# Kernel tuning notes

Hardware: AMD Instinct MI355X
Metric: run time of the kernel (lower is better)

## Reference

```python
import jax, jax.numpy as jnp
import numpy as np

EMBED_DIM = 1024
NUM_HEADS = 16
SEQ_LEN = 2048
BATCH = 2
LN_EPS = 1e-5


def setup_inputs() -> dict:
    key = jax.random.key(0)
    ks = jax.random.split(key, 12)
    d = EMBED_DIM
    s = 1.0 / np.sqrt(d)
    inp = {
        "x": jax.random.normal(ks[0], (BATCH, SEQ_LEN, d), dtype=jnp.float32),
        "ln1_g": jnp.ones((d,), jnp.float32),
        "ln1_b": jnp.zeros((d,), jnp.float32),
        "ln2_g": jnp.ones((d,), jnp.float32),
        "ln2_b": jnp.zeros((d,), jnp.float32),
        "W_qkv": jax.random.normal(ks[1], (d, 3 * d), jnp.float32) * s,
        "b_qkv": jnp.zeros((3 * d,), jnp.float32),
        "W_proj": jax.random.normal(ks[2], (d, d), jnp.float32) * s,
        "b_proj": jnp.zeros((d,), jnp.float32),
        "W_fc": jax.random.normal(ks[3], (d, 4 * d), jnp.float32) * s,
        "b_fc": jnp.zeros((4 * d,), jnp.float32),
        "W_out": jax.random.normal(ks[4], (4 * d, d), jnpp_dummy := jnp.float32) * (1.0 / np.sqrt(4 * d)),
        "b_out": jnp.zeros((d,), jnp.float32),
    }
    return inp


def _layernorm(x, g, b):
    mu = jnp.mean(x, axis=-1, keepdims=True)
    var = jnp.mean(jnp.square(x - mu), axis=-1, keepdims=True)
    return (x - mu) * jax.lax.rsqrt(var + LN_EPS) * g + b


def _block(x, ln1_g, ln1_b, ln2_g, ln2_b, W_qkv, b_qkv, W_proj, b_proj, W_fc, b_fc, W_out, b_out):
    B, S, D = x.shape
    H = NUM_HEADS
    hd = D // H
    h = _layernorm(x, ln1_g, ln1_b)
    qkv = h @ W_qkv + b_qkv  # [B,S,3D]
    q, k, v = jnp.split(qkv, 3, axis=-1)
    # [B,H,S,hd]
    q = q.reshape(B, S, H, hd).transpose(0, 2, 1, 3)
    k = k.reshape(B, S, H, hd).transpose(0, 2, 1, 3)
    v = v.reshape(B, S, H, hd).transpose(0, 2, 1, 3)
    attn = jnp.einsum("bhqd,bhkd->bhqk", q, k) / np.sqrt(hd).astype(np.float32)
    causal = jnp.tril(jnp.ones((S, S), dtype=bool))
    attn = jnp.where(causal, attn, -jnp.inf)
    attn = jax.nn.softmax(attn, axis=-1)
    y = jnp.einsum("bhqk,bhkd->bhqd", attn, v)
    y = y.transpose(0, 2, 1, 3).reshape(B, S, D)
    y = y @ W_proj + b_proj
    x = x + y
    h2 = _layernorm(x, ln2_g, ln2_b)
    m = jax.nn.relu(h2 @ W_fc + b_fc) @ W_out + b_out
    return x + m


def reference(x, ln1_g, ln1_b, ln2_g, ln2_b, W_qkv, b_qkv, W_proj, b_proj, W_fc, b_fc, W_out, b_out):
    return _block(x, ln1_g, ln1_b, ln2_g, ln2_b, W_qkv, b_qkv, W_proj, b_proj, W_fc, b_fc, W_out, b_out)
```

## Files before the change

### kernel.cpp

```cpp
#include <hip/hip_runtime.h>

typedef unsigned short u16;
typedef __attribute__((ext_vector_type(8))) __bf16 bf16x8;
typedef __attribute__((ext_vector_type(4))) float f32x4;

#define DEV __device__ __forceinline__

DEV u16 f2bf(float f) {
  unsigned u = __float_as_uint(f);
  u += 0x7fffu + ((u >> 16) & 1u);
  return (u16)(u >> 16);
}
DEV float bf2f(u16 u) { return __uint_as_float((unsigned)u << 16); }

DEV void gl_lds16(const void* g, void* l) {
  __builtin_amdgcn_global_load_lds(
      (const __attribute__((address_space(1))) void*)(uintptr_t)g,
      (__attribute__((address_space(3))) void*)(unsigned)(uintptr_t)l, 16, 0, 0);
}

DEV float wave_sum64(float v) {
#pragma unroll
  for (int off = 32; off > 0; off >>= 1) v += __shfl_down(v, off);
  return v;
}

__global__ __launch_bounds__(256) void ln_kernel(const float* __restrict__ x,
                                                 const float* __restrict__ g,
                                                 const float* __restrict__ be,
                                                 u16* __restrict__ out) {
  const int row = blockIdx.x, t = threadIdx.x;
  const int w = t >> 6, L = t & 63;
  __shared__ float red[8];
  const float4 v = reinterpret_cast<const float4*>(x + (size_t)row * 1024)[t];
  float s = v.x + v.y + v.z + v.w;
  s = wave_sum64(s);
  if (L == 0) red[w] = s;
  __syncthreads();
  const float mean = (red[0] + red[1] + red[2] + red[3]) * (1.0f / 1024.0f);
  const float dx = v.x - mean, dy = v.y - mean, dz = v.z - mean, dw = v.w - mean;
  float q = dx * dx + dy * dy + dz * dz + dw * dw;
  q = wave_sum64(q);
  if (L == 0) red[4 + w] = q;
  __syncthreads();
  const float var = (red[4] + red[5] + red[6] + red[7]) * (1.0f / 1024.0f);
  const float rs = rsqrtf(var + 1e-5f);
  const float4 gg = reinterpret_cast<const float4*>(g)[t];
  const float4 bb = reinterpret_cast<const float4*>(be)[t];
  ushort4 o;
  o.x = f2bf(dx * rs * gg.x + bb.x);
  o.y = f2bf(dy * rs * gg.y + bb.y);
  o.z = f2bf(dz * rs * gg.z + bb.z);
  o.w = f2bf(dw * rs * gg.w + bb.w);
  reinterpret_cast<ushort4*>(out + (size_t)row * 1024)[t] = o;
}

__global__ __launch_bounds__(256) void proj_reduce_ln(const float* __restrict__ x,
                                                      const float* __restrict__ bias,
                                                      const float* __restrict__ P,
                                                      const float* __restrict__ g,
                                                      const float* __restrict__ be,
                                                      float* __restrict__ x2,
                                                      u16* __restrict__ hbuf) {
  constexpr size_t MN = (size_t)4096 * 1024;
  const int row = blockIdx.x, t = threadIdx.x;
  const int w = t >> 6, L = t & 63;
  __shared__ float red[8];
  const float4 xv = reinterpret_cast<const float4*>(x + (size_t)row * 1024)[t];
  const float4 bv = reinterpret_cast<const float4*>(bias)[t];
  const float4 p0 = reinterpret_cast<const float4*>(P + (size_t)row * 1024)[t];
  const float4 p1 = reinterpret_cast<const float4*>(P + MN + (size_t)row * 1024)[t];
  float4 v;
  v.x = xv.x + bv.x + p0.x + p1.x;
  v.y = xv.y + bv.y + p0.y + p1.y;
  v.z = xv.z + bv.z + p0.z + p1.z;
  v.w = xv.w + bv.w + p0.w + p1.w;
  reinterpret_cast<float4*>(x2 + (size_t)row * 1024)[t] = v;
  float s = v.x + v.y + v.z + v.w;
  s = wave_sum64(s);
  if (L == 0) red[w] = s;
  __syncthreads();
  const float mean = (red[0] + red[1] + red[2] + red[3]) * (1.0f / 1024.0f);
  const float dx = v.x - mean, dy = v.y - mean, dz = v.z - mean, dw = v.w - mean;
  float q = dx * dx + dy * dy + dz * dz + dw * dw;
  q = wave_sum64(q);
  if (L == 0) red[4 + w] = q;
  __syncthreads();
  const float var = (red[4] + red[5] + red[6] + red[7]) * (1.0f / 1024.0f);
  const float rs = rsqrtf(var + 1e-5f);
  const float4 gg = reinterpret_cast<const float4*>(g)[t];
  const float4 bb = reinterpret_cast<const float4*>(be)[t];
  ushort4 o;
  o.x = f2bf(dx * rs * gg.x + bb.x);
  o.y = f2bf(dy * rs * gg.y + bb.y);
  o.z = f2bf(dz * rs * gg.z + bb.z);
  o.w = f2bf(dw * rs * gg.w + bb.w);
  reinterpret_cast<ushort4*>(hbuf + (size_t)row * 1024)[t] = o;
}

__global__ __launch_bounds__(256) void out_reduce(const float* __restrict__ x2,
                                                  const float* __restrict__ bias,
                                                  const u16* __restrict__ P0,
                                                  const u16* __restrict__ P1,
                                                  const u16* __restrict__ P2,
                                                  const u16* __restrict__ P3,
                                                  float* __restrict__ dout) {
  const int row = blockIdx.x, t = threadIdx.x;
  const size_t off = (size_t)row * 1024;
  const float4 xv = reinterpret_cast<const float4*>(x2 + off)[t];
  const float4 bv = reinterpret_cast<const float4*>(bias)[t];
  const ushort4 a = reinterpret_cast<const ushort4*>(P0 + off)[t];
  const ushort4 b = reinterpret_cast<const ushort4*>(P1 + off)[t];
  const ushort4 c = reinterpret_cast<const ushort4*>(P2 + off)[t];
  const ushort4 d = reinterpret_cast<const ushort4*>(P3 + off)[t];
  float4 o;
  o.x = xv.x + bv.x + bf2f(a.x) + bf2f(b.x) + bf2f(c.x) + bf2f(d.x);
  o.y = xv.y + bv.y + bf2f(a.y) + bf2f(b.y) + bf2f(c.y) + bf2f(d.y);
  o.z = xv.z + bv.z + bf2f(a.z) + bf2f(b.z) + bf2f(c.z) + bf2f(d.z);
  o.w = xv.w + bv.w + bf2f(a.w) + bf2f(b.w) + bf2f(c.w) + bf2f(d.w);
  reinterpret_cast<float4*>(dout + off)[t] = o;
}

__global__ __launch_bounds__(256) void transpose_cvt(const float* __restrict__ W,
                                                     u16* __restrict__ Wt, int K, int N) {
  __shared__ float tile[32][33];
  const int c0 = blockIdx.x * 32, r0 = blockIdx.y * 32;
  const int tx = threadIdx.x & 31, ty = threadIdx.x >> 5;
#pragma unroll
  for (int j = 0; j < 4; ++j)
    tile[ty + j * 8][tx] = W[(size_t)(r0 + ty + j * 8) * N + c0 + tx];
  __syncthreads();
#pragma unroll
  for (int j = 0; j < 4; ++j) {
    const int n = c0 + ty + j * 8, k = r0 + tx;
    Wt[(size_t)n * K + k] = f2bf(tile[tx][ty + j * 8]);
  }
}

__global__ __launch_bounds__(256) void transpose_v(const u16* __restrict__ qkv,
                                                   u16* __restrict__ Vt) {
  __shared__ __attribute__((aligned(16))) u16 tile[64][72];
  const int s0 = blockIdx.x * 64;
  const int h = blockIdx.y, b = blockIdx.z;
  const int t = threadIdx.x;
#pragma unroll
  for (int i = 0; i < 2; ++i) {
    const int idx = i * 256 + t, r = idx >> 3, c = (idx & 7) << 3;
    const uint4 v =
        *(const uint4*)(qkv + (size_t)(b * 2048 + s0 + r) * 3072 + 2048 + h * 64 + c);
    *(uint4*)&tile[r][c] = v;
  }
  __syncthreads();
#pragma unroll
  for (int i = 0; i < 2; ++i) {
    const int idx = i * 256 + t, d = idx >> 3, sc = (idx & 7) << 3;
    u16 tmp[8];
#pragma unroll
    for (int j = 0; j < 8; ++j) tmp[j] = tile[sc + j][d];
    *(uint4*)(Vt + (size_t)((b * 16 + h) * 64 + d) * 2048 + s0 + sc) = *(uint4*)tmp;
  }
}

enum { F_BIAS = 1, F_RESID = 2, F_RELU = 4, F_BF16 = 8, F_SLICED = 16, F_PART4 = 32 };

template <int FLAGS>
__global__ __launch_bounds__(256, 2) void gemm_bt(const u16* __restrict__ A,
                                                  const u16* __restrict__ Bt,
                                                  const float* __restrict__ bias,
                                                  const float* __restrict__ resid,
                                                  void* __restrict__ Cout,
                                                  u16* __restrict__ pp0, u16* __restrict__ pp1,
                                                  u16* __restrict__ pp2, u16* __restrict__ pp3,
                                                  int M, int N, int K, int Kst) {
  __shared__ __attribute__((aligned(16))) u16 sA[128 * 32];
  __shared__ __attribute__((aligned(16))) u16 sB[128 * 32];
  const int t = threadIdx.x, w = t >> 6, L = t & 63, quad = L >> 4, l15 = L & 15;
  const int wm = w >> 1, wn = w & 1;
  const int m0 = blockIdx.y * 128, n0 = blockIdx.x * 128;
  const u16* Ag = A + (size_t)m0 * Kst + (size_t)blockIdx.z * K;
  const u16* Bg = Bt + (size_t)n0 * Kst + (size_t)blockIdx.z * K;

  f32x4 acc[4][4] = {};

  for (int k0 = 0; k0 < K; k0 += 32) {
    __syncthreads();
#pragma unroll
    for (int i = 0; i < 2; ++i) {
      const int cp = i * 256 + t, rr = cp >> 2, cc = (cp & 3) << 3;
      gl_lds16(Ag + (size_t)rr * Kst + k0 + cc, &sA[(i * 256 + w * 64) * 8]);
    }
#pragma unroll
    for (int i = 0; i < 2; ++i) {
      const int cp = i * 256 + t, rr = cp >> 2, cc = (cp & 3) << 3;
      gl_lds16(Bg + (size_t)rr * Kst + k0 + cc, &sB[(i * 256 + w * 64) * 8]);
    }
    __syncthreads();

    bf16x8 af[4], bfr[4];
#pragma unroll
    for (int m = 0; m < 4; ++m)
      af[m] = *(const bf16x8*)&sA[(wm * 64 + m * 16 + l15) * 32 + quad * 8];
#pragma unroll
    for (int n = 0; n < 4; ++n)
      bfr[n] = *(const bf16x8*)&sB[(wn * 64 + n * 16 + l15) * 32 + quad * 8];
#pragma unroll
    for (int m = 0; m < 4; ++m)
#pragma unroll
      for (int n = 0; n < 4; ++n)
        acc[m][n] = __builtin_amdgcn_mfma_f32_16x16x32_bf16(af[m], bfr[n], acc[m][n], 0, 0, 0);
  }

  u16* pbase = nullptr;
  if (FLAGS & F_PART4)
    pbase = (blockIdx.z == 0) ? pp0 : (blockIdx.z == 1) ? pp1 : (blockIdx.z == 2) ? pp2 : pp3;
  float* sbase = nullptr;
  if (FLAGS & F_SLICED) sbase = (float*)Cout + (size_t)blockIdx.z * M * N;

#pragma unroll
  for (int m = 0; m < 4; ++m) {
#pragma unroll
    for (int n = 0; n < 4; ++n) {
      const int col = n0 + wn * 64 + n * 16 + l15;
      const float bv = (FLAGS & F_BIAS) ? bias[col] : 0.0f;
#pragma unroll
      for (int rr = 0; rr < 4; ++rr) {
        const int row = m0 + wm * 64 + m * 16 + quad * 4 + rr;
        if (FLAGS & F_PART4) {
          pbase[(size_t)row * N + col] = f2bf(acc[m][n][rr]);
        } else if (FLAGS & F_SLICED) {
          sbase[(size_t)row * N + col] = acc[m][n][rr];
        } else {
          float v = acc[m][n][rr] + bv;
          if (FLAGS & F_RESID) v += resid[(size_t)row * N + col];
          if (FLAGS & F_RELU) v = fmaxf(v, 0.0f);
          if (FLAGS & F_BF16)
            ((u16*)Cout)[(size_t)row * N + col] = f2bf(v);
          else
            ((float*)Cout)[(size_t)row * N + col] = v;
        }
      }
    }
  }
}

__global__ __launch_bounds__(256) void flash_attn(const u16* __restrict__ qkv,
                                                  const u16* __restrict__ Vt,
                                                  u16* __restrict__ y) {
  constexpr int S = 2048, D3 = 3072, D = 1024;
  constexpr float Csc = 0.125f * 1.44269504088896f;
  __shared__ __attribute__((aligned(16))) u16 sK[2 * 64 * 32];
  __shared__ __attribute__((aligned(16))) u16 sV[2 * 64 * 32];
  __shared__ __attribute__((aligned(16))) u16 sP[4][2 * 16 * 40];

  const int lin = blockIdx.x;
  const int half = lin >> 9, rem = lin & 511;
  const int qt = half ? (31 - (rem & 31)) : (rem & 31);
  const int bh = (rem >> 5) | (half << 4);
  const int b = bh >> 4, h = bh & 15;
  const int q0 = qt * 64;

  const int t = threadIdx.x, w = t >> 6, L = t & 63, quad = L >> 4, l15 = L & 15;
  const int qw = q0 + w * 16;

  const u16* qbase = qkv + (size_t)(b * S) * D3 + h * 64;
  const u16* Kbase = qbase + D;
  const u16* Vbase = Vt + (size_t)((b * 16 + h) * 64) * S;

  bf16x8 aQ[2];
#pragma unroll
  for (int kk = 0; kk < 2; ++kk)
    aQ[kk] = *(const bf16x8*)(qbase + (size_t)(qw + l15) * D3 + kk * 32 + quad * 8);

  bf16x8 ones;
#pragma unroll
  for (int i = 0; i < 8; ++i) ones[i] = (__bf16)1.0f;

  f32x4 acc[4] = {};
  f32x4 lacc = {};

  u16* sPw = sP[w];
  const int nkv = qt + 1;
  for (int it = 0; it < nkv; ++it) {
    const int kv0 = it * 64;
    __syncthreads();
#pragma unroll
    for (int i = 0; i < 2; ++i) {
      const int cp = i * 256 + t;
      const int kk = cp >> 8, r = (cp >> 2) & 63, col = (cp & 3) << 3;
      gl_lds16(Kbase + (size_t)(kv0 + r) * D3 + kk * 32 + col, &sK[(i * 256 + w * 64) * 8]);
    }
#pragma unroll
    for (int i = 0; i < 2; ++i) {
      const int cp = i * 256 + t;
      const int kk = cp >> 8, d = (cp >> 2) & 63, col = (cp & 3) << 3;
      gl_lds16(Vbase + (size_t)d * S + kv0 + kk * 32 + col, &sV[(i * 256 + w * 64) * 8]);
    }
    __syncthreads();

    f32x4 s[4] = {};
#pragma unroll
    for (int kk = 0; kk < 2; ++kk) {
#pragma unroll
      for (int n = 0; n < 4; ++n) {
        const bf16x8 bK = *(const bf16x8*)&sK[kk * 2048 + (n * 16 + l15) * 32 + quad * 8];
        s[n] = __builtin_amdgcn_mfma_f32_16x16x32_bf16(aQ[kk], bK, s[n], 0, 0, 0);
      }
    }

    if (kv0 + 63 > qw) {
#pragma unroll
      for (int n = 0; n < 4; ++n) {
        const int col = kv0 + n * 16 + l15;
#pragma unroll
        for (int r = 0; r < 4; ++r) {
          const int row = qw + quad * 4 + r;
          const float p = __builtin_amdgcn_exp2f(s[n][r] * Csc);
          s[n][r] = (col > row) ? 0.0f : p;
        }
      }
    } else {
#pragma unroll
      for (int n = 0; n < 4; ++n)
#pragma unroll
        for (int r = 0; r < 4; ++r) s[n][r] = __builtin_amdgcn_exp2f(s[n][r] * Csc);
    }

#pragma unroll
    for (int n = 0; n < 4; ++n)
#pragma unroll
      for (int r = 0; r < 4; ++r)
        sPw[(n >> 1) * 640 + (quad * 4 + r) * 40 + (n & 1) * 16 + l15] = f2bf(s[n][r]);

#pragma unroll
    for (int kk = 0; kk < 2; ++kk) {
      const bf16x8 aP = *(const bf16x8*)&sPw[kk * 640 + l15 * 40 + quad * 8];
      lacc = __builtin_amdgcn_mfma_f32_16x16x32_bf16(aP, ones, lacc, 0, 0, 0);
#pragma unroll
      for (int dn = 0; dn < 4; ++dn) {
        const bf16x8 bV = *(const bf16x8*)&sV[kk * 2048 + (dn * 16 + l15) * 32 + quad * 8];
        acc[dn] = __builtin_amdgcn_mfma_f32_16x16x32_bf16(aP, bV, acc[dn], 0, 0, 0);
      }
    }
  }

#pragma unroll
  for (int r = 0; r < 4; ++r) {
    const float inv = 1.0f / lacc[r];
    const int row = qw + quad * 4 + r;
    u16* yb = y + (size_t)(b * S + row) * D + h * 64 + l15;
#pragma unroll
    for (int dn = 0; dn < 4; ++dn) yb[dn * 16] = f2bf(acc[dn][r] * inv);
  }
}

extern "C" void kernel_launch(void* const* d_in, const int* in_sizes, int n_in,
                              void* d_out, int out_size, void* d_ws, size_t ws_size,
                              hipStream_t stream) {
  const float* x = (const float*)d_in[0];
  const float* ln1g = (const float*)d_in[1];
  const float* ln1b = (const float*)d_in[2];
  const float* ln2g = (const float*)d_in[3];
  const float* ln2b = (const float*)d_in[4];
  const float* Wqkv = (const float*)d_in[5];
  const float* bqkv = (const float*)d_in[6];
  const float* Wproj = (const float*)d_in[7];
  const float* bproj = (const float*)d_in[8];
  const float* Wfc = (const float*)d_in[9];
  const float* bfc = (const float*)d_in[10];
  const float* Wout = (const float*)d_in[11];
  const float* bout = (const float*)d_in[12];

  char* ws = (char*)d_ws;
  const size_t MB = 1u << 20;
  u16* wt_out = (u16*)(ws + 0 * MB);
  u16* hbuf = (u16*)(ws + 8 * MB);
  float* x2 = (float*)(ws + 16 * MB);
  u16* ybuf = (u16*)(ws + 32 * MB);
  u16* qkvb = (u16*)(ws + 40 * MB);
  u16* vtb = (u16*)(ws + 64 * MB);
  u16* wt_qkv = (u16*)(ws + 72 * MB);
  u16* wt_proj = (u16*)(ws + 78 * MB);
  u16* wt_fc = (u16*)(ws + 80 * MB);
  float* projP = (float*)(ws + 40 * MB);
  u16* m1 = (u16*)(ws + 40 * MB);
  u16* po0 = (u16*)(ws + 8 * MB);
  u16* po1 = (u16*)(ws + 32 * MB);
  u16* po2 = (u16*)(ws + 72 * MB);
  u16* po3 = (u16*)(ws + 80 * MB);

  transpose_cvt<<<dim3(96, 32), 256, 0, stream>>>(Wqkv, wt_qkv, 1024, 3072);
  transpose_cvt<<<dim3(32, 32), 256, 0, stream>>>(Wproj, wt_proj, 1024, 1024);
  transpose_cvt<<<dim3(128, 32), 256, 0, stream>>>(Wfc, wt_fc, 1024, 4096);
  transpose_cvt<<<dim3(32, 128), 256, 0, stream>>>(Wout, wt_out, 4096, 1024);

  ln_kernel<<<4096, 256, 0, stream>>>(x, ln1g, ln1b, hbuf);
  gemm_bt<F_BIAS | F_BF16><<<dim3(24, 32), 256, 0, stream>>>(
      hbuf, wt_qkv, bqkv, nullptr, qkvb, nullptr, nullptr, nullptr, nullptr, 4096, 3072, 1024, 1024);
  transpose_v<<<dim3(32, 16, 2), 256, 0, stream>>>(qkvb, vtb);
  flash_attn<<<1024, 256, 0, stream>>>(qkvb, vtb, ybuf);

  gemm_bt<F_SLICED><<<dim3(8, 32, 2), 256, 0, stream>>>(
      ybuf, wt_proj, nullptr, nullptr, projP, nullptr, nullptr, nullptr, nullptr, 4096, 1024, 512, 1024);
  proj_reduce_ln<<<4096, 256, 0, stream>>>(x, bproj, projP, ln2g, ln2b, x2, hbuf);

  gemm_bt<F_BIAS | F_RELU | F_BF16><<<dim3(32, 32), 256, 0, stream>>>(
      hbuf, wt_fc, bfc, nullptr, m1, nullptr, nullptr, nullptr, nullptr, 4096, 4096, 1024, 1024);

  gemm_bt<F_PART4><<<dim3(8, 32, 4), 256, 0, stream>>>(
      m1, wt_out, nullptr, nullptr, nullptr, po0, po1, po2, po3, 4096, 1024, 1024, 4096);
  out_reduce<<<4096, 256, 0, stream>>>(x2, bout, po0, po1, po2, po3, (float*)d_out);
}
```

Before: 355.9 us.

## Merge weight transposes with LN1 into one kernel and double GEMM K-step

Replaces the four weight transpose/convert launches and the LN1 kernel with a single prep kernel that dispatches on block index, cutting launch overhead and the gaps between small kernels. The GEMM main loop now stages 64 K-elements per iteration in two LDS halves, so it hits half as many barriers per unit of K. The GEMM change doubles LDS per block (32 KB), which could limit occupancy, and the merged kernel uses a 33x32 float shared buffer even for the LN blocks.

```diff
diff --git a/kernel.cpp b/kernel.cpp
--- a/kernel.cpp
+++ b/kernel.cpp
@@ -25,14 +25,9 @@
   return v;
 }
 
-__global__ __launch_bounds__(256) void ln_kernel(const float* __restrict__ x,
-                                                 const float* __restrict__ g,
-                                                 const float* __restrict__ be,
-                                                 u16* __restrict__ out) {
-  const int row = blockIdx.x, t = threadIdx.x;
+DEV void ln_body(const float4 v, const float* g, const float* be, u16* out_row, int t,
+                 float* red) {
   const int w = t >> 6, L = t & 63;
-  __shared__ float red[8];
-  const float4 v = reinterpret_cast<const float4*>(x + (size_t)row * 1024)[t];
   float s = v.x + v.y + v.z + v.w;
   s = wave_sum64(s);
   if (L == 0) red[w] = s;
@@ -52,7 +47,49 @@
   o.y = f2bf(dy * rs * gg.y + bb.y);
   o.z = f2bf(dz * rs * gg.z + bb.z);
   o.w = f2bf(dw * rs * gg.w + bb.w);
-  reinterpret_cast<ushort4*>(out + (size_t)row * 1024)[t] = o;
+  reinterpret_cast<ushort4*>(out_row)[t] = o;
+}
+
+__global__ __launch_bounds__(256) void prep_kernel(
+    const float* __restrict__ x, const float* __restrict__ ln1g,
+    const float* __restrict__ ln1b, u16* __restrict__ hbuf,
+    const float* __restrict__ Wqkv, u16* __restrict__ wt_qkv,
+    const float* __restrict__ Wproj, u16* __restrict__ wt_proj,
+    const float* __restrict__ Wfc, u16* __restrict__ wt_fc,
+    const float* __restrict__ Wout, u16* __restrict__ wt_out) {
+  __shared__ float smem[32 * 33];
+  int id = blockIdx.x;
+  const int t = threadIdx.x;
+  if (id < 4096) {
+    const float4 v = reinterpret_cast<const float4*>(x + (size_t)id * 1024)[t];
+    ln_body(v, ln1g, ln1b, hbuf + (size_t)id * 1024, t, smem);
+    return;
+  }
+  id -= 4096;
+  const float* W;
+  u16* Wt;
+  int K, N, nbx;
+  if (id < 3072) {
+    W = Wqkv; Wt = wt_qkv; K = 1024; N = 3072; nbx = 96;
+  } else if (id < 3072 + 1024) {
+    id -= 3072; W = Wproj; Wt = wt_proj; K = 1024; N = 1024; nbx = 32;
+  } else if (id < 3072 + 1024 + 4096) {
+    id -= 3072 + 1024; W = Wfc; Wt = wt_fc; K = 1024; N = 4096; nbx = 128;
+  } else {
+    id -= 3072 + 1024 + 4096; W = Wout; Wt = wt_out; K = 4096; N = 1024; nbx = 32;
+  }
+  float(*tile)[33] = (float(*)[33])smem;
+  const int c0 = (id % nbx) * 32, r0 = (id / nbx) * 32;
+  const int tx = t & 31, ty = t >> 5;
+#pragma unroll
+  for (int j = 0; j < 4; ++j)
+    tile[ty + j * 8][tx] = W[(size_t)(r0 + ty + j * 8) * N + c0 + tx];
+  __syncthreads();
+#pragma unroll
+  for (int j = 0; j < 4; ++j) {
+    const int n = c0 + ty + j * 8, k = r0 + tx;
+    Wt[(size_t)n * K + k] = f2bf(tile[tx][ty + j * 8]);
+  }
 }
 
 __global__ __launch_bounds__(256) void proj_reduce_ln(const float* __restrict__ x,
@@ -64,7 +101,6 @@
                                                       u16* __restrict__ hbuf) {
   constexpr size_t MN = (size_t)4096 * 1024;
   const int row = blockIdx.x, t = threadIdx.x;
-  const int w = t >> 6, L = t & 63;
   __shared__ float red[8];
   const float4 xv = reinterpret_cast<const float4*>(x + (size_t)row * 1024)[t];
   const float4 bv = reinterpret_cast<const float4*>(bias)[t];
@@ -76,26 +112,7 @@
   v.z = xv.z + bv.z + p0.z + p1.z;
   v.w = xv.w + bv.w + p0.w + p1.w;
   reinterpret_cast<float4*>(x2 + (size_t)row * 1024)[t] = v;
-  float s = v.x + v.y + v.z + v.w;
-  s = wave_sum64(s);
-  if (L == 0) red[w] = s;
-  __syncthreads();
-  const float mean = (red[0] + red[1] + red[2] + red[3]) * (1.0f / 1024.0f);
-  const float dx = v.x - mean, dy = v.y - mean, dz = v.z - mean, dw = v.w - mean;
-  float q = dx * dx + dy * dy + dz * dz + dw * dw;
-  q = wave_sum64(q);
-  if (L == 0) red[4 + w] = q;
-  __syncthreads();
-  const float var = (red[4] + red[5] + red[6] + red[7]) * (1.0f / 1024.0f);
-  const float rs = rsqrtf(var + 1e-5f);
-  const float4 gg = reinterpret_cast<const float4*>(g)[t];
-  const float4 bb = reinterpret_cast<const float4*>(be)[t];
-  ushort4 o;
-  o.x = f2bf(dx * rs * gg.x + bb.x);
-  o.y = f2bf(dy * rs * gg.y + bb.y);
-  o.z = f2bf(dz * rs * gg.z + bb.z);
-  o.w = f2bf(dw * rs * gg.w + bb.w);
-  reinterpret_cast<ushort4*>(hbuf + (size_t)row * 1024)[t] = o;
+  ln_body(v, g, be, hbuf + (size_t)row * 1024, t, red);
 }
 
 __global__ __launch_bounds__(256) void out_reduce(const float* __restrict__ x2,
@@ -121,22 +138,6 @@
   reinterpret_cast<float4*>(dout + off)[t] = o;
 }
 
-__global__ __launch_bounds__(256) void transpose_cvt(const float* __restrict__ W,
-                                                     u16* __restrict__ Wt, int K, int N) {
-  __shared__ float tile[32][33];
-  const int c0 = blockIdx.x * 32, r0 = blockIdx.y * 32;
-  const int tx = threadIdx.x & 31, ty = threadIdx.x >> 5;
-#pragma unroll
-  for (int j = 0; j < 4; ++j)
-    tile[ty + j * 8][tx] = W[(size_t)(r0 + ty + j * 8) * N + c0 + tx];
-  __syncthreads();
-#pragma unroll
-  for (int j = 0; j < 4; ++j) {
-    const int n = c0 + ty + j * 8, k = r0 + tx;
-    Wt[(size_t)n * K + k] = f2bf(tile[tx][ty + j * 8]);
-  }
-}
-
 __global__ __launch_bounds__(256) void transpose_v(const u16* __restrict__ qkv,
                                                    u16* __restrict__ Vt) {
   __shared__ __attribute__((aligned(16))) u16 tile[64][72];
@@ -172,8 +173,8 @@
                                                   u16* __restrict__ pp0, u16* __restrict__ pp1,
                                                   u16* __restrict__ pp2, u16* __restrict__ pp3,
                                                   int M, int N, int K, int Kst) {
-  __shared__ __attribute__((aligned(16))) u16 sA[128 * 32];
-  __shared__ __attribute__((aligned(16))) u16 sB[128 * 32];
+  __shared__ __attribute__((aligned(16))) u16 sA[2][128 * 32];
+  __shared__ __attribute__((aligned(16))) u16 sB[2][128 * 32];
   const int t = threadIdx.x, w = t >> 6, L = t & 63, quad = L >> 4, l15 = L & 15;
   const int wm = w >> 1, wn = w & 1;
   const int m0 = blockIdx.y * 128, n0 = blockIdx.x * 128;
@@ -182,32 +183,39 @@
 
   f32x4 acc[4][4] = {};
 
-  for (int k0 = 0; k0 < K; k0 += 32) {
+  for (int k0 = 0; k0 < K; k0 += 64) {
     __syncthreads();
 #pragma unroll
-    for (int i = 0; i < 2; ++i) {
-      const int cp = i * 256 + t, rr = cp >> 2, cc = (cp & 3) << 3;
-      gl_lds16(Ag + (size_t)rr * Kst + k0 + cc, &sA[(i * 256 + w * 64) * 8]);
-    }
-#pragma unroll
-    for (int i = 0; i < 2; ++i) {
-      const int cp = i * 256 + t, rr = cp >> 2, cc = (cp & 3) << 3;
-      gl_lds16(Bg + (size_t)rr * Kst + k0 + cc, &sB[(i * 256 + w * 64) * 8]);
+    for (int h = 0; h < 2; ++h) {
+#pragma unroll
+      for (int i = 0; i < 2; ++i) {
+        const int cp = i * 256 + t, rr = cp >> 2, cc = (cp & 3) << 3;
+        gl_lds16(Ag + (size_t)rr * Kst + k0 + h * 32 + cc, &sA[h][(i * 256 + w * 64) * 8]);
+      }
+#pragma unroll
+      for (int i = 0; i < 2; ++i) {
+        const int cp = i * 256 + t, rr = cp >> 2, cc = (cp & 3) << 3;
+        gl_lds16(Bg + (size_t)rr * Kst + k0 + h * 32 + cc, &sB[h][(i * 256 + w * 64) * 8]);
+      }
     }
     __syncthreads();
 
-    bf16x8 af[4], bfr[4];
-#pragma unroll
-    for (int m = 0; m < 4; ++m)
-      af[m] = *(const bf16x8*)&sA[(wm * 64 + m * 16 + l15) * 32 + quad * 8];
-#pragma unroll
-    for (int n = 0; n < 4; ++n)
-      bfr[n] = *(const bf16x8*)&sB[(wn * 64 + n * 16 + l15) * 32 + quad * 8];
-#pragma unroll
-    for (int m = 0; m < 4; ++m)
+#pragma unroll
+    for (int h = 0; h < 2; ++h) {
+      bf16x8 af[4], bfr[4];
+#pragma unroll
+      for (int m = 0; m < 4; ++m)
+        af[m] = *(const bf16x8*)&sA[h][(wm * 64 + m * 16 + l15) * 32 + quad * 8];
 #pragma unroll
       for (int n = 0; n < 4; ++n)
-        acc[m][n] = __builtin_amdgcn_mfma_f32_16x16x32_bf16(af[m], bfr[n], acc[m][n], 0, 0, 0);
+        bfr[n] = *(const bf16x8*)&sB[h][(wn * 64 + n * 16 + l15) * 32 + quad * 8];
+#pragma unroll
+      for (int m = 0; m < 4; ++m)
+#pragma unroll
+        for (int n = 0; n < 4; ++n)
+          acc[m][n] =
+              __builtin_amdgcn_mfma_f32_16x16x32_bf16(af[m], bfr[n], acc[m][n], 0, 0, 0);
+    }
   }
 
   u16* pbase = nullptr;
@@ -388,12 +396,9 @@
   u16* po2 = (u16*)(ws + 72 * MB);
   u16* po3 = (u16*)(ws + 80 * MB);
 
-  transpose_cvt<<<dim3(96, 32), 256, 0, stream>>>(Wqkv, wt_qkv, 1024, 3072);
-  transpose_cvt<<<dim3(32, 32), 256, 0, stream>>>(Wproj, wt_proj, 1024, 1024);
-  transpose_cvt<<<dim3(128, 32), 256, 0, stream>>>(Wfc, wt_fc, 1024, 4096);
-  transpose_cvt<<<dim3(32, 128), 256, 0, stream>>>(Wout, wt_out, 4096, 1024);
-
-  ln_kernel<<<4096, 256, 0, stream>>>(x, ln1g, ln1b, hbuf);
+  prep_kernel<<<4096 + 3072 + 1024 + 4096 + 4096, 256, 0, stream>>>(
+      x, ln1g, ln1b, hbuf, Wqkv, wt_qkv, Wproj, wt_proj, Wfc, wt_fc, Wout, wt_out);
+
   gemm_bt<F_BIAS | F_BF16><<<dim3(24, 32), 256, 0, stream>>>(
       hbuf, wt_qkv, bqkv, nullptr, qkvb, nullptr, nullptr, nullptr, nullptr, 4096, 3072, 1024, 1024);
   transpose_v<<<dim3(32, 16, 2), 256, 0, stream>>>(qkvb, vtb);
```

New measurement: 340.0 us. 4.5% less time.
